# Kernel tuning notes

Hardware: AMD Instinct MI355X
Metric: run time of the kernel (lower is better)

## Reference

```python
import jax, jax.numpy as jnp
import numpy as np

IN_F, H1, H2, NC = 784, 1024, 1024, 10
BATCH = 32
EPS = 0.1


def setup_inputs() -> dict:
    key = jax.random.key(0)
    ks = jax.random.split(key, 8)
    x = jax.random.normal(ks[0], (BATCH, IN_F), jnp.float32)
    y = jax.random.randint(ks[1], (BATCH,), 0, NC)
    W1 = jax.random.normal(ks[2], (H1, IN_F), jnp.float32) / np.float32(np.sqrt(IN_F))
    b1 = jax.random.normal(ks[3], (H1,), jnp.float32) * 0.01
    W2 = jax.random.normal(ks[4], (H2, H1), jnp.float32) / np.float32(np.sqrt(H1))
    b2 = jax.random.normal(ks[5], (H2,), jnp.float32) * 0.01
    W3 = jax.random.normal(ks[6], (NC, H2), jnp.float32) / np.float32(np.sqrt(H2))
    b3 = jax.random.normal(ks[7], (NC,), jnp.float32) * 0.01
    return dict(x=x, y=y, W1=W1, b1=b1, W2=W2, b2=b2, W3=W3, b3=b3)


def _relu_coeffs(zl, zu):
    # d = 1 where zl>=0, zu/(zu-zl) where crossing, 0 where zu<=0 (as in select_layer)
    I = (zl < 0) & (zu > 0)
    d = jnp.where(zl >= 0, 1.0, jnp.where(I, zu / (zu - zl), 0.0))
    lI = jnp.where(I, zl, 0.0)  # zl restricted to crossing set I
    return d, lI


def reference(x, y, W1, b1, W2, b2, W3, b3):
    eps = jnp.float32(EPS)
    # ---- layer-1 preactivation bounds (InfBall fval) ----
    nom1 = x @ W1.T + b1                              # [B,H1]
    r1 = eps * jnp.abs(W1).sum(1)                     # [H1]
    zl1, zu1 = nom1 - r1, nom1 + r1
    d1, l1m = _relu_coeffs(zl1, zu1)                  # [B,H1]

    # ---- layer-2 preactivation bounds via dual (transpose) propagation, nu = I ----
    nu1 = W2[None, :, :] * d1[:, None, :]             # [B,H2,H1]  (D1 W2^T rows)
    V0 = jnp.einsum('bji,ik->bjk', nu1, W1)           # [B,H2,IN]
    A = jnp.einsum('bjk,bk->bj', V0, x) + b2 + nu1 @ b1
    E = eps * jnp.abs(V0).sum(-1)
    crossl = jnp.einsum('bji,bi->bj', jax.nn.relu(-nu1), l1m)
    crossu = jnp.einsum('bji,bi->bj', jax.nn.relu(nu1), l1m)
    zl2 = A - E + crossl
    zu2 = A + E - crossu
    d2, l2m = _relu_coeffs(zl2, zu2)                  # [B,H2]

    # ---- final robust bounds: c[b,j,:] = e_{y_b} - e_j ----
    eye = jnp.eye(NC, dtype=x.dtype)
    c = eye[y][:, None, :] - eye[None, :, :]          # [B,NC,NC]
    nu2 = (c @ W3) * d2[:, None, :]                   # [B,NC,H2]
    nu1f = (nu2 @ W2) * d1[:, None, :]                # [B,NC,H1]
    V0f = nu1f @ W1                                   # [B,NC,IN]
    Af = jnp.einsum('bjk,bk->bj', V0f, x) + c @ b3 + nu2 @ b2 + nu1f @ b1
    Ef = eps * jnp.abs(V0f).sum(-1)
    crossf = (jnp.einsum('bji,bi->bj', jax.nn.relu(-nu2), l2m)
              + jnp.einsum('bji,bi->bj', jax.nn.relu(-nu1f), l1m))
    J = Af - Ef + crossf                              # lower bound of c^T z
    return -J                                         # f: upper bound of z_j - z_y, [B,NC]
```

## Files before the change

### kernel.cpp

```cpp
#include <hip/hip_runtime.h>
#include <math.h>

#define B    32
#define INF  784
#define H1   1024
#define H2   1024
#define NC   10
#define EPSV 0.1f

typedef __attribute__((ext_vector_type(8))) short short8;
typedef __attribute__((ext_vector_type(4))) float floatx4;

__device__ inline ushort bf16_rne(float f) {
  uint u = __builtin_bit_cast(uint, f);
  u += 0x7FFFu + ((u >> 16) & 1u);
  return (ushort)(u >> 16);
}
__device__ inline uint pack2(float a, float b) {
  return (uint)bf16_rne(a) | ((uint)bf16_rne(b) << 16);
}
__device__ inline uint scale_pack(uint u, float d0, float d1v) {
  float f0 = __builtin_bit_cast(float, u << 16) * d0;
  float f1 = __builtin_bit_cast(float, u & 0xFFFF0000u) * d1v;
  uint r0 = __builtin_bit_cast(uint, f0) + 0x8000u;
  uint r1 = __builtin_bit_cast(uint, f1) + 0x8000u;
  return __builtin_amdgcn_perm(r1, r0, 0x07060302u);
}

__global__ __launch_bounds__(256) void k_pre(
    const float* __restrict__ x, const float* __restrict__ W1,
    const float* __restrict__ b1, const float* __restrict__ W2,
    ushort* __restrict__ W1F, ushort* __restrict__ W2F,
    float* __restrict__ d1B, float* __restrict__ t1B, float* __restrict__ dnB,
    float* __restrict__ Ezero)
{
  __shared__ float red[4][B + 1];
  __shared__ float Ts[4][32][17];
  int bid = blockIdx.x;
  int t = threadIdx.x;
  if (bid < 64) {
    int jt = bid;
    int lane = t & 63, c0 = t >> 6;
    int l15 = lane & 15, quad = lane >> 4;
    for (int c = c0; c < 32; c += 4) {
      const float* src = &W2[(size_t)(jt * 16 + l15) * H1 + c * 32 + quad * 8];
      float4 v0 = *reinterpret_cast<const float4*>(src);
      float4 v1 = *reinterpret_cast<const float4*>(src + 4);
      uint4 o;
      o.x = pack2(v0.x, v0.y); o.y = pack2(v0.z, v0.w);
      o.z = pack2(v1.x, v1.y); o.w = pack2(v1.z, v1.w);
      *reinterpret_cast<uint4*>(&W2F[((size_t)(c * 64 + jt) * 64 + lane) * 8]) = o;
    }
  } else if (bid < 113) {
    int mt = bid - 64;
    int col0 = mt * 16;
    int w = t >> 6, lane = t & 63;
    int l15 = lane & 15, quad = lane >> 4;
    for (int cg = 0; cg < 8; cg++) {
      int c = cg * 4 + w;
#pragma unroll
      for (int p = 0; p < 8; p++) {
        int r = p * 4 + (lane >> 4);
        Ts[w][r][lane & 15] = W1[(size_t)(c * 32 + r) * INF + col0 + (lane & 15)];
      }
      float f[8];
#pragma unroll
      for (int e = 0; e < 8; e++) f[e] = Ts[w][quad * 8 + e][l15];
      uint4 o;
      o.x = pack2(f[0], f[1]); o.y = pack2(f[2], f[3]);
      o.z = pack2(f[4], f[5]); o.w = pack2(f[6], f[7]);
      *reinterpret_cast<uint4*>(&W1F[((size_t)(c * 49 + mt) * 64 + lane) * 8]) = o;
    }
  } else if (bid < 1137) {
    int i = bid - 113;
    const float* w = W1 + (size_t)i * INF;
    float acc[B];
#pragma unroll
    for (int b = 0; b < B; b++) acc[b] = 0.f;
    float wabs = 0.f;
    for (int k = t; k < INF; k += 256) {
      float wv = w[k];
      wabs += fabsf(wv);
#pragma unroll
      for (int b = 0; b < B; b++) acc[b] = fmaf(x[b * INF + k], wv, acc[b]);
    }
#pragma unroll
    for (int off = 32; off > 0; off >>= 1) {
#pragma unroll
      for (int b = 0; b < B; b++) acc[b] += __shfl_down(acc[b], off, 64);
      wabs += __shfl_down(wabs, off, 64);
    }
    int wave = t >> 6, lane = t & 63;
    if (lane == 0) {
#pragma unroll
      for (int b = 0; b < B; b++) red[wave][b] = acc[b];
      red[wave][B] = wabs;
    }
    __syncthreads();
    if (t < B) {
      float s = red[0][t] + red[1][t] + red[2][t] + red[3][t];
      float r = EPSV * (red[0][B] + red[1][B] + red[2][B] + red[3][B]);
      float nom = s + b1[i];
      float zl = nom - r, zu = nom + r;
      float d, l;
      if (zl >= 0.f)      { d = 1.f;            l = 0.f; }
      else if (zu > 0.f)  { d = zu / (zu - zl); l = zl;  }
      else                { d = 0.f;            l = 0.f; }
      d1B[(size_t)t * H1 + i] = d;
      t1B[(size_t)t * H1 + i] = d * l;
      dnB[(size_t)t * H1 + i] = d * nom;
    }
  } else {
    int zb = bid - 1137;
    for (int idx = t; idx < 8192; idx += 256) {
      int pos = zb * 8192 + idx;
      if (pos < 54272) Ezero[pos] = 0.f;
    }
  }
}

#define K3_LOAD(c, A, Bv) do {                                                  \
  _Pragma("unroll")                                                             \
  for (int ni = 0; ni < 2; ni++)                                                \
    Bv[ni] = *reinterpret_cast<const uint4*>(bBase + (size_t)(c) * 32768 + ni * 512); \
  _Pragma("unroll")                                                             \
  for (int mi = 0; mi < 7; mi++)                                                \
    A[mi] = *reinterpret_cast<const uint4*>(aBase + (size_t)(c) * 25088 + mi * 512); \
} while (0)

#define K3F_COMP(c, A, Bv) do {                                                 \
  float4 dv0 = *reinterpret_cast<const float4*>(&Ds[(c) * 32 + quad * 8]);      \
  float4 dv1 = *reinterpret_cast<const float4*>(&Ds[(c) * 32 + quad * 8 + 4]);  \
  short8 bfr[2];                                                                \
  _Pragma("unroll")                                                             \
  for (int ni = 0; ni < 2; ni++) {                                              \
    uint4 sb;                                                                   \
    sb.x = scale_pack(Bv[ni].x, dv0.x, dv0.y);                                  \
    sb.y = scale_pack(Bv[ni].y, dv0.z, dv0.w);                                  \
    sb.z = scale_pack(Bv[ni].z, dv1.x, dv1.y);                                  \
    sb.w = scale_pack(Bv[ni].w, dv1.z, dv1.w);                                  \
    bfr[ni] = __builtin_bit_cast(short8, sb);                                   \
  }                                                                             \
  _Pragma("unroll")                                                             \
  for (int mi = 0; mi < 7; mi++) {                                              \
    short8 af = __builtin_bit_cast(short8, A[mi]);                              \
    _Pragma("unroll")                                                           \
    for (int ni = 0; ni < 2; ni++)                                              \
      acc[mi][ni] = __builtin_amdgcn_mfma_f32_16x16x32_bf16(af, bfr[ni], acc[mi][ni], 0, 0, 0); \
  }                                                                             \
} while (0)

__global__ __launch_bounds__(256, 3) void k3(
    const ushort* __restrict__ W1F, const ushort* __restrict__ W2F,
    const float* __restrict__ d1B, float* __restrict__ E)
{
  int b = blockIdx.z;
  int t = threadIdx.x, w = t >> 6, lane = t & 63;
  int quad = lane >> 4, l15 = lane & 15;
  int mt0 = blockIdx.x * 7;
  int jt0 = blockIdx.y * 8 + w * 2;

  __shared__ float Ds[H1];
  for (int idx = t; idx < H1; idx += 256) Ds[idx] = d1B[(size_t)b * H1 + idx];
  __syncthreads();

  const ushort* aBase = W1F + ((size_t)mt0 * 64 + lane) * 8;
  const ushort* bBase = W2F + ((size_t)jt0 * 64 + lane) * 8;

  floatx4 acc[7][2];
#pragma unroll
  for (int mi = 0; mi < 7; mi++)
#pragma unroll
    for (int ni = 0; ni < 2; ni++) acc[mi][ni] = (floatx4){0.f, 0.f, 0.f, 0.f};

  uint4 a0[7], b0[2], a1[7], b1v[2];
  K3_LOAD(0, a0, b0);
  K3_LOAD(1, a1, b1v);
  for (int c = 0; c < 30; c += 2) {
    K3F_COMP(c, a0, b0);
    K3_LOAD(c + 2, a0, b0);
    K3F_COMP(c + 1, a1, b1v);
    if (c + 3 < 32) K3_LOAD(c + 3, a1, b1v);
  }
  K3F_COMP(30, a0, b0);
  K3F_COMP(31, a1, b1v);

#pragma unroll
  for (int ni = 0; ni < 2; ni++) {
    float s = 0.f;
#pragma unroll
    for (int mi = 0; mi < 7; mi++)
#pragma unroll
      for (int r = 0; r < 4; r++) s += fabsf(acc[mi][ni][r]);
    s += __shfl_xor(s, 16, 64);
    s += __shfl_xor(s, 32, 64);
    if (lane < 16) {
      int j = (jt0 + ni) * 16 + l15;
      atomicAdd(&E[(size_t)j * B + b], EPSV * s);
    }
  }
}

__global__ __launch_bounds__(256) void k245a(
    const float* __restrict__ W2, const float* __restrict__ b2,
    const float* __restrict__ dnB, const float* __restrict__ t1B,
    const float* __restrict__ E, const float* __restrict__ W3,
    const int* __restrict__ y,
    float* __restrict__ nu2T, float* __restrict__ F2)
{
  int j = blockIdx.x;
  int t = threadIdx.x;
  int wave = t >> 6, lane = t & 63;
  int b0 = wave * 8;
  float aA[8] = {}, aCl[8] = {}, aCu[8] = {};
  const float* __restrict__ w2 = W2 + (size_t)j * H1;
  for (int i = lane; i < H1; i += 64) {
    float wv = w2[i];
    float wp = fmaxf(wv, 0.f), wn = fmaxf(-wv, 0.f);
#pragma unroll
    for (int r = 0; r < 8; r++) {
      float dv = dnB[(size_t)(b0 + r) * H1 + i];
      float tv = t1B[(size_t)(b0 + r) * H1 + i];
      aA[r]  = fmaf(wv, dv, aA[r]);
      aCl[r] = fmaf(wn, tv, aCl[r]);
      aCu[r] = fmaf(wp, tv, aCu[r]);
    }
  }
#pragma unroll
  for (int off = 32; off > 0; off >>= 1) {
#pragma unroll
    for (int r = 0; r < 8; r++) {
      aA[r]  += __shfl_down(aA[r],  off, 64);
      aCl[r] += __shfl_down(aCl[r], off, 64);
      aCu[r] += __shfl_down(aCu[r], off, 64);
    }
  }
  __shared__ float sA[B], sCl[B], sCu[B];
  __shared__ float sd2[B], st2[B], sdb[B], swy[B], sw3[NC];
  float bj = b2[j];
  if (lane == 0) {
#pragma unroll
    for (int r = 0; r < 8; r++) {
      sA [b0 + r] = aA[r] + bj;
      sCl[b0 + r] = aCl[r];
      sCu[b0 + r] = aCu[r];
    }
  }
  if (t >= 64 && t < 96)   swy[t - 64]  = W3[(size_t)y[t - 64] * H2 + j];
  if (t >= 128 && t < 138) sw3[t - 128] = W3[(size_t)(t - 128) * H2 + j];
  __syncthreads();
  if (t < B) {
    float a = sA[t], e = E[(size_t)j * B + t];
    float zl = a - e + sCl[t];
    float zu = a + e - sCu[t];
    float d, l;
    if (zl >= 0.f)      { d = 1.f;            l = 0.f; }
    else if (zu > 0.f)  { d = zu / (zu - zl); l = zl;  }
    else                { d = 0.f;            l = 0.f; }
    sd2[t] = d;
    st2[t] = d * l;
    sdb[t] = d * bj;
  }
  __syncthreads();
  for (int tt = t; tt < B * NC; tt += 256) {
    int b = tt / NC, jc = tt - b * NC;
    float cw = swy[b] - sw3[jc];
    float d2v = sd2[b];
    nu2T[((size_t)b * H2 + j) * 12 + jc] = cw * d2v;
    float val = cw * sdb[b] + fmaxf(-cw, 0.f) * st2[b];
    atomicAdd(&F2[((size_t)(j & 63) * B + b) * NC + jc], val);
  }
}

__global__ __launch_bounds__(256) void k5b1(
    const float* __restrict__ W2, const float* __restrict__ nu2T,
    float* __restrict__ hpart)
{
  int t = threadIdx.x;
  int i1 = blockIdx.x * 512 + t * 2;
  int b = blockIdx.y, s = blockIdx.z;
  const float* __restrict__ nrowb = nu2T + ((size_t)b * H2 + s * 128) * 12;
  const float* __restrict__ w2b = W2 + (size_t)s * 128 * H1 + i1;
  float h0[NC] = {}, h1[NC] = {};
  for (int i2 = 0; i2 < 128; i2++) {
    float2 wv = *reinterpret_cast<const float2*>(&w2b[(size_t)i2 * H1]);
    const float* __restrict__ nrow = nrowb + i2 * 12;
#pragma unroll
    for (int j = 0; j < NC; j++) {
      h0[j] = fmaf(nrow[j], wv.x, h0[j]);
      h1[j] = fmaf(nrow[j], wv.y, h1[j]);
    }
  }
#pragma unroll
  for (int j = 0; j < NC; j++) {
    float2 o; o.x = h0[j]; o.y = h1[j];
    *reinterpret_cast<float2*>(&hpart[(((size_t)s * B + b) * NC + j) * H1 + i1]) = o;
  }
}

__global__ __launch_bounds__(256) void k5b2(
    const float* __restrict__ hpart,
    const float* __restrict__ d1B, const float* __restrict__ t1B,
    const float* __restrict__ dnB,
    float* __restrict__ nu1fT, float* __restrict__ F)
{
  int t = threadIdx.x;
  int i1 = blockIdx.x * 256 + t;
  int b = blockIdx.y;
  float d1v = d1B[(size_t)b * H1 + i1];
  float t1v = t1B[(size_t)b * H1 + i1];
  float dnv = dnB[(size_t)b * H1 + i1];
  float sn[NC], c1[NC];
#pragma unroll
  for (int j = 0; j < NC; j++) {
    float hv = 0.f;
#pragma unroll
    for (int s = 0; s < 8; s++)
      hv += hpart[(((size_t)s * B + b) * NC + j) * H1 + i1];
    nu1fT[((size_t)b * H1 + i1) * 12 + j] = hv * d1v;
    sn[j] = hv * dnv;
    c1[j] = fmaxf(-hv, 0.f) * t1v;
  }
#pragma unroll
  for (int off = 32; off > 0; off >>= 1) {
#pragma unroll
    for (int j = 0; j < NC; j++) {
      sn[j] += __shfl_down(sn[j], off, 64);
      c1[j] += __shfl_down(c1[j], off, 64);
    }
  }
  __shared__ float red[4][2 * NC];
  int wave = t >> 6, lane = t & 63;
  if (lane == 0) {
#pragma unroll
    for (int j = 0; j < NC; j++) { red[wave][j] = sn[j]; red[wave][NC + j] = c1[j]; }
  }
  __syncthreads();
  if (t < NC) {
    float s = 0.f;
    for (int w = 0; w < 4; w++) s += red[w][t] + red[w][NC + t];
    atomicAdd(&F[b * NC + t], s);
  }
}

__global__ __launch_bounds__(128) void k5c1(
    const float* __restrict__ W1, const float* __restrict__ nu1fT,
    float* __restrict__ ppart)
{
  int t = threadIdx.x;
  bool valid = (t < 112);
  int k = blockIdx.x * 112 + (valid ? t : 0);
  int b = blockIdx.y, s = blockIdx.z;
  const float* __restrict__ nrowb = nu1fT + ((size_t)b * H1 + s * 128) * 12;
  const float* __restrict__ w1b = W1 + (size_t)s * 128 * INF + k;
  float acc[NC] = {};
  for (int i1 = 0; i1 < 128; i1++) {
    float w1v = w1b[(size_t)i1 * INF];
    const float* __restrict__ nrow = nrowb + i1 * 12;
#pragma unroll
    for (int j = 0; j < NC; j++) acc[j] = fmaf(nrow[j], w1v, acc[j]);
  }
  if (valid) {
#pragma unroll
    for (int j = 0; j < NC; j++)
      ppart[(((size_t)s * B + b) * NC + j) * INF + k] = acc[j];
  }
}

__global__ __launch_bounds__(256) void k5c2_out(
    const float* __restrict__ ppart, const float* __restrict__ F,
    const float* __restrict__ F2, const float* __restrict__ b3,
    const int* __restrict__ y, float* __restrict__ out)
{
  int b = blockIdx.x;
  int t = threadIdx.x;
  float e[NC] = {};
  for (int k = t; k < INF; k += 256) {
#pragma unroll
    for (int j = 0; j < NC; j++) {
      float v = 0.f;
#pragma unroll
      for (int s = 0; s < 8; s++)
        v += ppart[(((size_t)s * B + b) * NC + j) * INF + k];
      e[j] += fabsf(v);
    }
  }
#pragma unroll
  for (int off = 32; off > 0; off >>= 1) {
#pragma unroll
    for (int j = 0; j < NC; j++) e[j] += __shfl_down(e[j], off, 64);
  }
  __shared__ float red[4][NC];
  int wave = t >> 6, lane = t & 63;
  if (lane == 0) {
#pragma unroll
    for (int j = 0; j < NC; j++) red[wave][j] = e[j];
  }
  __syncthreads();
  if (t < NC) {
    float ef = 0.f;
    for (int w = 0; w < 4; w++) ef += red[w][t];
    float s = F[b * NC + t];
    for (int slot = 0; slot < 64; slot++)
      s += F2[((size_t)slot * B + b) * NC + t];
    int yb = y[b];
    s += b3[yb] - b3[t];
    out[b * NC + t] = EPSV * ef - s;
  }
}

extern "C" void kernel_launch(void* const* d_in, const int* in_sizes, int n_in,
                              void* d_out, int out_size, void* d_ws, size_t ws_size,
                              hipStream_t stream) {
  const float* x  = (const float*)d_in[0];
  const int*   y  = (const int*)  d_in[1];
  const float* W1 = (const float*)d_in[2];
  const float* b1 = (const float*)d_in[3];
  const float* W2 = (const float*)d_in[4];
  const float* b2 = (const float*)d_in[5];
  const float* W3 = (const float*)d_in[6];
  const float* b3 = (const float*)d_in[7];
  float* out = (float*)d_out;
  float* ws  = (float*)d_ws;

  float* d1B  = ws;
  float* t1B  = ws + 32768;
  float* dnB  = ws + 65536;
  float* E    = ws + 196608;
  float* F    = ws + 229376;
  float* F2   = ws + 230400;
  float* nu2T = ws + 328704;
  ushort* W2F = (ushort*)(ws + 721920);
  ushort* W1F = (ushort*)(ws + 1246208);
  float* nu1fT = ws + 328704;
  float* hpart = ws + 721920;
  float* ppart = ws + 721920;

  k_pre<<<1144, 256, 0, stream>>>(x, W1, b1, W2, W1F, W2F, d1B, t1B, dnB, E);
  k3<<<dim3(7, 8, 32), 256, 0, stream>>>(W1F, W2F, d1B, E);
  k245a<<<H2, 256, 0, stream>>>(W2, b2, dnB, t1B, E, W3, y, nu2T, F2);
  k5b1<<<dim3(2, B, 8), 256, 0, stream>>>(W2, nu2T, hpart);
  k5b2<<<dim3(4, B), 256, 0, stream>>>(hpart, d1B, t1B, dnB, nu1fT, F);
  k5c1<<<dim3(7, B, 8), 128, 0, stream>>>(W1, nu1fT, ppart);
  k5c2_out<<<B, 256, 0, stream>>>(ppart, F, F2, b3, y, out);
}
```

Before: 225.1 us.

## Process two batch items per k3 block to reuse W1/W2 tile loads

Each k3 block now handles two batch elements, loading the shared W1F/W2F bf16 tiles once and applying both batches' d1 scales to run two sets of MFMA accumulators. This halves global tile traffic and the grid size. In exchange it doubles accumulator registers, lowering the occupancy hint from 3 to 2 waves per SIMD, and launches fewer blocks.

Measured after the change: 213.2 us. 1.06x faster.

```diff
diff --git a/kernel.cpp b/kernel.cpp
--- a/kernel.cpp
+++ b/kernel.cpp
@@ -128,9 +128,9 @@
     A[mi] = *reinterpret_cast<const uint4*>(aBase + (size_t)(c) * 25088 + mi * 512); \
 } while (0)
 
-#define K3F_COMP(c, A, Bv) do {                                                 \
-  float4 dv0 = *reinterpret_cast<const float4*>(&Ds[(c) * 32 + quad * 8]);      \
-  float4 dv1 = *reinterpret_cast<const float4*>(&Ds[(c) * 32 + quad * 8 + 4]);  \
+#define K3F_COMP(c, A, Bv, DsRow, accB) do {                                    \
+  float4 dv0 = *reinterpret_cast<const float4*>(&DsRow[(c) * 32]);              \
+  float4 dv1 = *reinterpret_cast<const float4*>(&DsRow[(c) * 32 + 4]);          \
   short8 bfr[2];                                                                \
   _Pragma("unroll")                                                             \
   for (int ni = 0; ni < 2; ni++) {                                              \
@@ -146,57 +146,69 @@
     short8 af = __builtin_bit_cast(short8, A[mi]);                              \
     _Pragma("unroll")                                                           \
     for (int ni = 0; ni < 2; ni++)                                              \
-      acc[mi][ni] = __builtin_amdgcn_mfma_f32_16x16x32_bf16(af, bfr[ni], acc[mi][ni], 0, 0, 0); \
+      accB[mi][ni] = __builtin_amdgcn_mfma_f32_16x16x32_bf16(af, bfr[ni], accB[mi][ni], 0, 0, 0); \
   }                                                                             \
 } while (0)
 
-__global__ __launch_bounds__(256, 3) void k3(
+__global__ __launch_bounds__(256, 2) void k3(
     const ushort* __restrict__ W1F, const ushort* __restrict__ W2F,
     const float* __restrict__ d1B, float* __restrict__ E)
 {
-  int b = blockIdx.z;
+  int b0 = blockIdx.z * 2;
   int t = threadIdx.x, w = t >> 6, lane = t & 63;
   int quad = lane >> 4, l15 = lane & 15;
   int mt0 = blockIdx.x * 7;
   int jt0 = blockIdx.y * 8 + w * 2;
 
-  __shared__ float Ds[H1];
-  for (int idx = t; idx < H1; idx += 256) Ds[idx] = d1B[(size_t)b * H1 + idx];
+  __shared__ float Ds[2][H1];
+  for (int idx = t; idx < 2 * H1; idx += 256)
+    Ds[idx >> 10][idx & 1023] = d1B[(size_t)(b0 + (idx >> 10)) * H1 + (idx & 1023)];
   __syncthreads();
 
   const ushort* aBase = W1F + ((size_t)mt0 * 64 + lane) * 8;
   const ushort* bBase = W2F + ((size_t)jt0 * 64 + lane) * 8;
-
-  floatx4 acc[7][2];
-#pragma unroll
-  for (int mi = 0; mi < 7; mi++)
-#pragma unroll
-    for (int ni = 0; ni < 2; ni++) acc[mi][ni] = (floatx4){0.f, 0.f, 0.f, 0.f};
-
-  uint4 a0[7], b0[2], a1[7], b1v[2];
-  K3_LOAD(0, a0, b0);
+  const float* Ds0 = &Ds[0][quad * 8];
+  const float* Ds1 = &Ds[1][quad * 8];
+
+  floatx4 acc[2][7][2];
+#pragma unroll
+  for (int bb = 0; bb < 2; bb++)
+#pragma unroll
+    for (int mi = 0; mi < 7; mi++)
+#pragma unroll
+      for (int ni = 0; ni < 2; ni++) acc[bb][mi][ni] = (floatx4){0.f, 0.f, 0.f, 0.f};
+
+  uint4 a0[7], b0v[2], a1[7], b1v[2];
+  K3_LOAD(0, a0, b0v);
   K3_LOAD(1, a1, b1v);
   for (int c = 0; c < 30; c += 2) {
-    K3F_COMP(c, a0, b0);
-    K3_LOAD(c + 2, a0, b0);
-    K3F_COMP(c + 1, a1, b1v);
+    K3F_COMP(c, a0, b0v, Ds0, acc[0]);
+    K3F_COMP(c, a0, b0v, Ds1, acc[1]);
+    K3_LOAD(c + 2, a0, b0v);
+    K3F_COMP(c + 1, a1, b1v, Ds0, acc[0]);
+    K3F_COMP(c + 1, a1, b1v, Ds1, acc[1]);
     if (c + 3 < 32) K3_LOAD(c + 3, a1, b1v);
   }
-  K3F_COMP(30, a0, b0);
-  K3F_COMP(31, a1, b1v);
-
-#pragma unroll
-  for (int ni = 0; ni < 2; ni++) {
-    float s = 0.f;
-#pragma unroll
-    for (int mi = 0; mi < 7; mi++)
-#pragma unroll
-      for (int r = 0; r < 4; r++) s += fabsf(acc[mi][ni][r]);
-    s += __shfl_xor(s, 16, 64);
-    s += __shfl_xor(s, 32, 64);
-    if (lane < 16) {
-      int j = (jt0 + ni) * 16 + l15;
-      atomicAdd(&E[(size_t)j * B + b], EPSV * s);
+  K3F_COMP(30, a0, b0v, Ds0, acc[0]);
+  K3F_COMP(30, a0, b0v, Ds1, acc[1]);
+  K3F_COMP(31, a1, b1v, Ds0, acc[0]);
+  K3F_COMP(31, a1, b1v, Ds1, acc[1]);
+
+#pragma unroll
+  for (int bb = 0; bb < 2; bb++) {
+#pragma unroll
+    for (int ni = 0; ni < 2; ni++) {
+      float s = 0.f;
+#pragma unroll
+      for (int mi = 0; mi < 7; mi++)
+#pragma unroll
+        for (int r = 0; r < 4; r++) s += fabsf(acc[bb][mi][ni][r]);
+      s += __shfl_xor(s, 16, 64);
+      s += __shfl_xor(s, 32, 64);
+      if (lane < 16) {
+        int j = (jt0 + ni) * 16 + l15;
+        atomicAdd(&E[(size_t)j * B + b0 + bb], EPSV * s);
+      }
     }
   }
 }
@@ -437,7 +449,7 @@
   float* ppart = ws + 721920;
 
   k_pre<<<1144, 256, 0, stream>>>(x, W1, b1, W2, W1F, W2F, d1B, t1B, dnB, E);
-  k3<<<dim3(7, 8, 32), 256, 0, stream>>>(W1F, W2F, d1B, E);
+  k3<<<dim3(7, 8, 16), 256, 0, stream>>>(W1F, W2F, d1B, E);
   k245a<<<H2, 256, 0, stream>>>(W2, b2, dnB, t1B, E, W3, y, nu2T, F2);
   k5b1<<<dim3(2, B, 8), 256, 0, stream>>>(W2, nu2T, hpart);
   k5b2<<<dim3(4, B), 256, 0, stream>>>(hpart, d1B, t1B, dnB, nu1fT, F);
```
